# Optimization experiments

Measured on AMD Instinct MI355X. Metric: run time of the kernel, lower is better.

Reference implementation:

```python
import jax, jax.numpy as jnp
import numpy as np

N = 50000
E = 600000
IN_DIM = 256
H1, H2, H3 = 128, 64, 64
HEADS = 8


def _add_self_loops(edge_index, edge_weight=None):
    loop = jnp.arange(N, dtype=edge_index.dtype)
    src = jnp.concatenate([edge_index[0], loop])
    dst = jnp.concatenate([edge_index[1], loop])
    if edge_weight is None:
        return src, dst, None
    ew = jnp.concatenate([edge_weight, jnp.ones((N,), edge_weight.dtype)])
    return src, dst, ew


def gcn_conv(x, edge_index, edge_weight, W, b):
    # PyG GCNConv: add self-loops (weight 1), symmetric normalization, scatter-add.
    src, dst, ew = _add_self_loops(edge_index, edge_weight)
    deg = jax.ops.segment_sum(ew, dst, num_segments=N)          # [N]
    dinv = jnp.where(deg > 0, jax.lax.rsqrt(jnp.maximum(deg, 1e-12)), 0.0)
    coeff = dinv[src] * ew * dinv[dst]                          # [E+N]
    h = x @ W                                                    # [N, out]
    out = jax.ops.segment_sum(coeff[:, None] * h[src], dst, num_segments=N)
    return out + b


def gat_conv(x, edge_index, W, att_src, att_dst, b):
    # PyG GATConv, heads=HEADS, concat=False (mean over heads), leaky_relu slope 0.2.
    src, dst, _ = _add_self_loops(edge_index)
    C = W.shape[1] // HEADS
    h = (x @ W).reshape(N, HEADS, C)                             # [N,H,C]
    a_s = jnp.sum(h * att_src, axis=-1)                          # [N,H]
    a_d = jnp.sum(h * att_dst, axis=-1)                          # [N,H]
    e = jax.nn.leaky_relu(a_s[src] + a_d[dst], negative_slope=0.2)  # [E',H]
    # scatter-softmax over edges sharing a destination
    m = jax.ops.segment_max(e, dst, num_segments=N)              # [N,H]
    p = jnp.exp(e - m[dst])
    s = jax.ops.segment_sum(p, dst, num_segments=N)              # [N,H]
    alpha = p / (s[dst] + 1e-16)                                 # [E',H]
    out = jax.ops.segment_sum(alpha[:, :, None] * h[src], dst, num_segments=N)  # [N,H,C]
    return jnp.mean(out, axis=1) + b


def setup_inputs() -> dict:
    key = jax.random.key(0)
    ks = jax.random.split(key, 12)
    x = jax.random.normal(ks[0], (N, IN_DIM), dtype=jnp.float32)
    edge_index = jax.random.randint(ks[1], (2, E), 0, N, dtype=jnp.int32)
    edge_weight = jax.random.uniform(ks[2], (E,), dtype=jnp.float32)
    def glorot(k, shape):
        fan = shape[0] + shape[-1]
        return jax.random.normal(k, shape, dtype=jnp.float32) * np.sqrt(2.0 / fan)
    return {
        "x": x, "edge_index": edge_index, "edge_weight": edge_weight,
        "gc1_w": glorot(ks[3], (IN_DIM, H1)), "gc1_b": jnp.zeros((H1,), jnp.float32),
        "gat_w": glorot(ks[4], (H1, HEADS * H2)),
        "att_src": glorot(ks[5], (HEADS, H2)), "att_dst": glorot(ks[6], (HEADS, H2)),
        "gat_b": jnp.zeros((H2,), jnp.float32),
        "gc2_w": glorot(ks[7], (H2, H3)), "gc2_b": jnp.zeros((H3,), jnp.float32),
        "fc_w": glorot(ks[8], (H3, 1)), "fc_b": jnp.zeros((1,), jnp.float32),
    }


def reference(x, edge_index, edge_weight, gc1_w, gc1_b, gat_w, att_src, att_dst,
              gat_b, gc2_w, gc2_b, fc_w, fc_b):
    # dropout is inference no-op
    h = jax.nn.relu(gcn_conv(x, edge_index, edge_weight, gc1_w, gc1_b))
    h = jax.nn.relu(gat_conv(h, edge_index, gat_w, att_src, att_dst, gat_b))
    h = jax.nn.relu(gcn_conv(h, edge_index, edge_weight, gc2_w, gc2_b))
    return h @ fc_w + fc_b                                       # [N,1]
```

## Files before the change

kernel.cpp:

```cpp
#include <hip/hip_runtime.h>
#include <hip/hip_bf16.h>

#define GNN_N 50000
#define GNN_E 600000

typedef unsigned int uint;
typedef unsigned short ushort;
using short8 = __attribute__((ext_vector_type(8))) short;
using f32x4  = __attribute__((ext_vector_type(4))) float;

__device__ __forceinline__ float leaky02(float x) { return x > 0.f ? x : 0.2f * x; }
__device__ __forceinline__ ushort f2b(float f) {
    uint u = __float_as_uint(f);
    return (ushort)((u + 0x7fffu + ((u >> 16) & 1u)) >> 16);
}
__device__ __forceinline__ float b2f(ushort b) { return __uint_as_float(((uint)b) << 16); }
__device__ __forceinline__ float blo(uint u) { return __uint_as_float(u << 16); }
__device__ __forceinline__ float bhi(uint u) { return __uint_as_float(u & 0xffff0000u); }

__global__ void gnn_hist(const int* __restrict__ dst, const float* __restrict__ ew,
                         int* __restrict__ cnt, float* __restrict__ deg, int e) {
    int i = blockIdx.x * blockDim.x + threadIdx.x;
    if (i >= e) return;
    int d = dst[i];
    atomicAdd(&cnt[d], 1);
    atomicAdd(&deg[d], ew[i]);
}
__global__ void gnn_deg_fin(float* deg, int n) {
    int i = blockIdx.x * blockDim.x + threadIdx.x;
    if (i < n) deg[i] = rsqrtf(1.0f + deg[i]);
}
__global__ void gnn_scan1(const int* __restrict__ cnt, int* __restrict__ row_ptr,
                          int* __restrict__ blksum, int n) {
    __shared__ int sh[256];
    int tid = threadIdx.x;
    int base = blockIdx.x * 1024 + tid * 4;
    int v0 = (base + 0 < n) ? cnt[base + 0] : 0;
    int v1 = (base + 1 < n) ? cnt[base + 1] : 0;
    int v2 = (base + 2 < n) ? cnt[base + 2] : 0;
    int v3 = (base + 3 < n) ? cnt[base + 3] : 0;
    int tsum = v0 + v1 + v2 + v3;
    sh[tid] = tsum;
    __syncthreads();
    for (int off = 1; off < 256; off <<= 1) {
        int t = (tid >= off) ? sh[tid - off] : 0;
        __syncthreads();
        sh[tid] += t;
        __syncthreads();
    }
    int excl = sh[tid] - tsum;
    if (base + 0 < n) row_ptr[base + 0] = excl; excl += v0;
    if (base + 1 < n) row_ptr[base + 1] = excl; excl += v1;
    if (base + 2 < n) row_ptr[base + 2] = excl; excl += v2;
    if (base + 3 < n) row_ptr[base + 3] = excl;
    if (tid == 255) blksum[blockIdx.x] = sh[255];
}
__global__ void gnn_scan2(int* blksum, int nblk, int* row_ptr_end, int total) {
    if (threadIdx.x == 0 && blockIdx.x == 0) {
        int run = 0;
        for (int b = 0; b < nblk; ++b) { int t = blksum[b]; blksum[b] = run; run += t; }
        *row_ptr_end = total;
    }
}
__global__ void gnn_scan3(int* row_ptr, const int* __restrict__ blksum, int n) {
    int i = blockIdx.x * blockDim.x + threadIdx.x;
    if (i < n) row_ptr[i] += blksum[i >> 10];
}
__global__ void gnn_scatter(const int* __restrict__ src, const int* __restrict__ dst,
                            const float* __restrict__ ew, const float* __restrict__ dinv,
                            const int* __restrict__ row_ptr, int* __restrict__ fill,
                            int* __restrict__ esrc, float* __restrict__ ecw, int e) {
    int i = blockIdx.x * blockDim.x + threadIdx.x;
    if (i >= e) return;
    int d = dst[i];
    int s = src[i];
    int pos = row_ptr[d] + atomicAdd(&fill[d], 1);
    esrc[pos] = s;
    ecw[pos] = dinv[s] * ew[i] * dinv[d];
}

__global__ void gnn_prep(const float* __restrict__ gc1_w, const float* __restrict__ gat_w,
                         const float* __restrict__ gc2_w, const float* __restrict__ att_src,
                         const float* __restrict__ att_dst, ushort* __restrict__ w1t,
                         ushort* __restrict__ w2s_t, ushort* __restrict__ w3t,
                         float* __restrict__ wa_t) {
    int t = blockIdx.x * 256 + threadIdx.x;
    if (t < 32768) {
        int k = t >> 7, n = t & 127;
        w1t[n * 256 + k] = f2b(gc1_w[t]);
        return;
    }
    t -= 32768;
    if (t < 65536) {
        int c = t >> 10, r = t & 1023;
        int h = r >> 7, k = r & 127;
        w2s_t[t] = f2b(0.125f * gat_w[(size_t)k * 512 + h * 64 + c]);
        return;
    }
    t -= 65536;
    if (t < 4096) {
        int k = t >> 6, n = t & 63;
        w3t[n * 64 + k] = f2b(gc2_w[t]);
        return;
    }
    t -= 4096;
    if (t < 2048) {
        int j = t >> 7, k = t & 127;
        int h = j & 7;
        const float* av = (j < 8) ? att_src : att_dst;
        float s = 0.f;
        for (int c = 0; c < 64; ++c) s += gat_w[(size_t)k * 512 + h * 64 + c] * av[h * 64 + c];
        wa_t[j * 128 + k] = s;
    }
}

template <bool AF32, bool BIAS>
__global__ __launch_bounds__(256) void gnn_mfma_gemm(const void* __restrict__ Av,
                                                     const ushort* __restrict__ Bt,
                                                     ushort* __restrict__ C,
                                                     const float* __restrict__ bias,
                                                     int M, int N, int K) {
    __shared__ ushort As[64 * 40];
    __shared__ ushort Bs[64 * 40];
    const int tid = threadIdx.x;
    const int wv = tid >> 6, lane = tid & 63;
    const int g = lane >> 4, r = lane & 15;
    const int brow = blockIdx.y << 6, bcol = blockIdx.x << 6;

    const int srow = tid >> 2;
    const int skoff = (tid & 3) << 3;
    int arow = brow + srow;
    if (arow >= M) arow = M - 1;
    const ushort* A16 = (const ushort*)Av;
    const float*  A32 = (const float*)Av;
    const ushort* Ap16 = A16 + (size_t)arow * K + skoff;
    const float*  Ap32 = A32 + (size_t)arow * K + skoff;
    const ushort* Bp = Bt + (size_t)(bcol + srow) * K + skoff;
    ushort* AsW = &As[srow * 40 + skoff];
    ushort* BsW = &Bs[srow * 40 + skoff];

    f32x4 acc[4] = {};

    for (int k0 = 0; k0 < K; k0 += 32) {
        if constexpr (AF32) {
            float4 f0 = *(const float4*)(Ap32 + k0);
            float4 f1 = *(const float4*)(Ap32 + k0 + 4);
            short8 t;
            t[0] = (short)f2b(f0.x); t[1] = (short)f2b(f0.y);
            t[2] = (short)f2b(f0.z); t[3] = (short)f2b(f0.w);
            t[4] = (short)f2b(f1.x); t[5] = (short)f2b(f1.y);
            t[6] = (short)f2b(f1.z); t[7] = (short)f2b(f1.w);
            *(short8*)AsW = t;
        } else {
            *(short8*)AsW = *(const short8*)(Ap16 + k0);
        }
        *(short8*)BsW = *(const short8*)(Bp + k0);
        __syncthreads();
        short8 bfrag = *(const short8*)&Bs[(wv * 16 + r) * 40 + g * 8];
#pragma unroll
        for (int mb = 0; mb < 4; ++mb) {
            short8 afrag = *(const short8*)&As[(mb * 16 + r) * 40 + g * 8];
            acc[mb] = __builtin_amdgcn_mfma_f32_16x16x32_bf16(afrag, bfrag, acc[mb], 0, 0, 0);
        }
        __syncthreads();
    }

    const int col = bcol + wv * 16 + r;
    float bv = 0.f;
    if constexpr (BIAS) bv = bias[col];
#pragma unroll
    for (int mb = 0; mb < 4; ++mb) {
        int rowb = brow + mb * 16 + g * 4;
#pragma unroll
        for (int rr = 0; rr < 4; ++rr) {
            int row = rowb + rr;
            if (row < M) {
                float val = acc[mb][rr];
                if constexpr (BIAS) {
                    val += bv;
                    val = val > 0.f ? val : 0.f;
                }
                C[(size_t)row * N + col] = f2b(val);
            }
        }
    }
}

__global__ __launch_bounds__(256) void gnn_gcn_node128_asd(const int* __restrict__ row_ptr,
                                                           const int* __restrict__ esrc,
                                                           const float* __restrict__ ecw,
                                                           const float* __restrict__ dinv,
                                                           const ushort* __restrict__ hb,
                                                           const float* __restrict__ b,
                                                           const float* __restrict__ wa,
                                                           ushort* __restrict__ out,
                                                           float* __restrict__ a_s,
                                                           float* __restrict__ a_d, int n) {
    __shared__ float swa[16 * 128];
    for (int i = threadIdx.x; i < 16 * 128; i += 256) swa[i] = wa[i];
    __syncthreads();
    int v = blockIdx.x * 4 + (threadIdx.x >> 6);
    int lane = threadIdx.x & 63;
    if (v >= n) return;
    const int sl = lane & 31;
    const int half = lane >> 5;
    float di = dinv[v];
    float a0, a1, a2, a3;
    {
        float scl = half ? 0.f : di * di;
        uint2 u = *(const uint2*)(hb + (size_t)v * 128 + 4 * sl);
        a0 = scl * blo(u.x); a1 = scl * bhi(u.x);
        a2 = scl * blo(u.y); a3 = scl * bhi(u.y);
    }
    int beg = row_ptr[v], end = row_ptr[v + 1];
    int cntE = end - beg;
    int pairs = cntE >> 1;
    int i = 0;
    for (; i + 4 <= pairs; i += 4) {
        int s[4]; float c[4]; uint2 u[4];
#pragma unroll
        for (int t = 0; t < 4; ++t) s[t] = esrc[beg + 2 * (i + t) + half];
#pragma unroll
        for (int t = 0; t < 4; ++t) c[t] = ecw[beg + 2 * (i + t) + half];
#pragma unroll
        for (int t = 0; t < 4; ++t) u[t] = *(const uint2*)(hb + (size_t)s[t] * 128 + 4 * sl);
#pragma unroll
        for (int t = 0; t < 4; ++t) {
            a0 += c[t] * blo(u[t].x); a1 += c[t] * bhi(u[t].x);
            a2 += c[t] * blo(u[t].y); a3 += c[t] * bhi(u[t].y);
        }
    }
    for (; i < pairs; ++i) {
        int s = esrc[beg + 2 * i + half];
        float c = ecw[beg + 2 * i + half];
        uint2 u = *(const uint2*)(hb + (size_t)s * 128 + 4 * sl);
        a0 += c * blo(u.x); a1 += c * bhi(u.x);
        a2 += c * blo(u.y); a3 += c * bhi(u.y);
    }
    if (cntE & 1) {
        int s = esrc[end - 1];
        float c = half ? 0.f : ecw[end - 1];
        uint2 u = *(const uint2*)(hb + (size_t)s * 128 + 4 * sl);
        a0 += c * blo(u.x); a1 += c * bhi(u.x);
        a2 += c * blo(u.y); a3 += c * bhi(u.y);
    }
    a0 += __shfl_xor(a0, 32); a1 += __shfl_xor(a1, 32);
    a2 += __shfl_xor(a2, 32); a3 += __shfl_xor(a3, 32);

    float4 bv = *(const float4*)(b + 4 * sl);
    float o0 = a0 + bv.x, o1 = a1 + bv.y, o2 = a2 + bv.z, o3 = a3 + bv.w;
    o0 = o0 > 0.f ? o0 : 0.f; o1 = o1 > 0.f ? o1 : 0.f;
    o2 = o2 > 0.f ? o2 : 0.f; o3 = o3 > 0.f ? o3 : 0.f;
    if (lane < 32) {
        uint2 w;
        w.x = (uint)f2b(o0) | ((uint)f2b(o1) << 16);
        w.y = (uint)f2b(o2) | ((uint)f2b(o3) << 16);
        *(uint2*)(out + (size_t)v * 128 + 4 * sl) = w;
    }

    float part[16];
#pragma unroll
    for (int j = 0; j < 16; ++j) {
        const float* wj = &swa[j * 128 + 4 * sl];
        part[j] = o0 * wj[0] + o1 * wj[1] + o2 * wj[2] + o3 * wj[3];
    }
#pragma unroll
    for (int m = 1; m < 32; m <<= 1) {
#pragma unroll
        for (int j = 0; j < 16; ++j) part[j] += __shfl_xor(part[j], m);
    }
    if (lane == 0) {
#pragma unroll
        for (int j = 0; j < 8; ++j) {
            a_s[(size_t)v * 8 + j] = part[j];
            a_d[(size_t)v * 8 + j] = part[8 + j];
        }
    }
}

__global__ __launch_bounds__(256) void gnn_gat_z(const int* __restrict__ row_ptr,
                                                 const int* __restrict__ esrc,
                                                 const float* __restrict__ a_s,
                                                 const float* __restrict__ a_d,
                                                 const ushort* __restrict__ g1b,
                                                 ushort* __restrict__ zb, int n) {
    int v = blockIdx.x * 4 + (threadIdx.x >> 6);
    int lane = threadIdx.x & 63;
    if (v >= n) return;
    const int sl = lane & 31;
    const int half = lane >> 5;
    const int hh = lane & 7;
    const int hbase = lane & 32;
    const float adh = a_d[(size_t)v * 8 + hh];

    float z0[8] = {}, z1[8] = {}, z2[8] = {}, z3[8] = {};
    float sloc = 0.f;
    {
        float pv = __expf(leaky02(a_s[(size_t)v * 8 + hh] + adh));
        if (half) pv = 0.f;
        sloc += pv;
        uint2 u = *(const uint2*)(g1b + (size_t)v * 128 + 4 * sl);
        float g0 = blo(u.x), g1v = bhi(u.x), g2v = blo(u.y), g3v = bhi(u.y);
        float ph[8];
#pragma unroll
        for (int h = 0; h < 8; ++h) ph[h] = __shfl(pv, hbase | h);
#pragma unroll
        for (int h = 0; h < 8; ++h) {
            z0[h] += ph[h] * g0; z1[h] += ph[h] * g1v;
            z2[h] += ph[h] * g2v; z3[h] += ph[h] * g3v;
        }
    }
    int beg = row_ptr[v], end = row_ptr[v + 1];
    int cntE = end - beg;
    int pairs = cntE >> 1;
    int i = 0;
    for (; i + 2 <= pairs; i += 2) {
        int s[2]; float e[2]; uint2 u[2];
#pragma unroll
        for (int t = 0; t < 2; ++t) s[t] = esrc[beg + 2 * (i + t) + half];
#pragma unroll
        for (int t = 0; t < 2; ++t) e[t] = a_s[(size_t)s[t] * 8 + hh];
#pragma unroll
        for (int t = 0; t < 2; ++t) u[t] = *(const uint2*)(g1b + (size_t)s[t] * 128 + 4 * sl);
#pragma unroll
        for (int t = 0; t < 2; ++t) {
            float pv = __expf(leaky02(e[t] + adh));
            sloc += pv;
            float g0 = blo(u[t].x), g1v = bhi(u[t].x), g2v = blo(u[t].y), g3v = bhi(u[t].y);
            float ph[8];
#pragma unroll
            for (int h = 0; h < 8; ++h) ph[h] = __shfl(pv, hbase | h);
#pragma unroll
            for (int h = 0; h < 8; ++h) {
                z0[h] += ph[h] * g0; z1[h] += ph[h] * g1v;
                z2[h] += ph[h] * g2v; z3[h] += ph[h] * g3v;
            }
        }
    }
    for (; i < pairs; ++i) {
        int s = esrc[beg + 2 * i + half];
        float pv = __expf(leaky02(a_s[(size_t)s * 8 + hh] + adh));
        sloc += pv;
        uint2 u = *(const uint2*)(g1b + (size_t)s * 128 + 4 * sl);
        float g0 = blo(u.x), g1v = bhi(u.x), g2v = blo(u.y), g3v = bhi(u.y);
        float ph[8];
#pragma unroll
        for (int h = 0; h < 8; ++h) ph[h] = __shfl(pv, hbase | h);
#pragma unroll
        for (int h = 0; h < 8; ++h) {
            z0[h] += ph[h] * g0; z1[h] += ph[h] * g1v;
            z2[h] += ph[h] * g2v; z3[h] += ph[h] * g3v;
        }
    }
    if (cntE & 1) {
        int s = esrc[end - 1];
        float pv = __expf(leaky02(a_s[(size_t)s * 8 + hh] + adh));
        if (half) pv = 0.f;
        sloc += pv;
        uint2 u = *(const uint2*)(g1b + (size_t)s * 128 + 4 * sl);
        float g0 = blo(u.x), g1v = bhi(u.x), g2v = blo(u.y), g3v = bhi(u.y);
        float ph[8];
#pragma unroll
        for (int h = 0; h < 8; ++h) ph[h] = __shfl(pv, hbase | h);
#pragma unroll
        for (int h = 0; h < 8; ++h) {
            z0[h] += ph[h] * g0; z1[h] += ph[h] * g1v;
            z2[h] += ph[h] * g2v; z3[h] += ph[h] * g3v;
        }
    }
    float slx = sloc + __shfl_xor(sloc, 32) + 1e-16f;
#pragma unroll
    for (int h = 0; h < 8; ++h) {
        z0[h] += __shfl_xor(z0[h], 32); z1[h] += __shfl_xor(z1[h], 32);
        z2[h] += __shfl_xor(z2[h], 32); z3[h] += __shfl_xor(z3[h], 32);
    }
    if (lane < 32) {
#pragma unroll
        for (int h = 0; h < 8; ++h) {
            float rs = 1.f / __shfl(slx, h);
            uint2 w;
            w.x = (uint)f2b(z0[h] * rs) | ((uint)f2b(z1[h] * rs) << 16);
            w.y = (uint)f2b(z2[h] * rs) | ((uint)f2b(z3[h] * rs) << 16);
            *(uint2*)(zb + (size_t)v * 1024 + h * 128 + 4 * sl) = w;
        }
    }
}

__global__ __launch_bounds__(256) void gnn_gcn_node64_fc(const int* __restrict__ row_ptr,
                                                         const int* __restrict__ esrc,
                                                         const float* __restrict__ ecw,
                                                         const float* __restrict__ dinv,
                                                         const ushort* __restrict__ hb,
                                                         const float* __restrict__ b,
                                                         const float* __restrict__ fc_w,
                                                         const float* __restrict__ fc_b,
                                                         float* __restrict__ out, int n) {
    int v = blockIdx.x * 4 + (threadIdx.x >> 6);
    int lane = threadIdx.x & 63;
    if (v >= n) return;
    const int sl = lane & 31;
    const int half = lane >> 5;
    float di = dinv[v];
    float a0, a1;
    {
        float scl = half ? 0.f : di * di;
        uint u = *(const uint*)(hb + (size_t)v * 64 + 2 * sl);
        a0 = scl * blo(u); a1 = scl * bhi(u);
    }
    int beg = row_ptr[v], end = row_ptr[v + 1];
    int cntE = end - beg;
    int pairs = cntE >> 1;
    int i = 0;
    for (; i + 4 <= pairs; i += 4) {
        int s[4]; float c[4]; uint u[4];
#pragma unroll
        for (int t = 0; t < 4; ++t) s[t] = esrc[beg + 2 * (i + t) + half];
#pragma unroll
        for (int t = 0; t < 4; ++t) c[t] = ecw[beg + 2 * (i + t) + half];
#pragma unroll
        for (int t = 0; t < 4; ++t) u[t] = *(const uint*)(hb + (size_t)s[t] * 64 + 2 * sl);
#pragma unroll
        for (int t = 0; t < 4; ++t) { a0 += c[t] * blo(u[t]); a1 += c[t] * bhi(u[t]); }
    }
    for (; i < pairs; ++i) {
        int s = esrc[beg + 2 * i + half];
        float c = ecw[beg + 2 * i + half];
        uint u = *(const uint*)(hb + (size_t)s * 64 + 2 * sl);
        a0 += c * blo(u); a1 += c * bhi(u);
    }
    if (cntE & 1) {
        int s = esrc[end - 1];
        float c = half ? 0.f : ecw[end - 1];
        uint u = *(const uint*)(hb + (size_t)s * 64 + 2 * sl);
        a0 += c * blo(u); a1 += c * bhi(u);
    }
    a0 += __shfl_xor(a0, 32);
    a1 += __shfl_xor(a1, 32);
    float o0 = a0 + b[2 * sl];
    float o1 = a1 + b[2 * sl + 1];
    o0 = o0 > 0.f ? o0 : 0.f;
    o1 = o1 > 0.f ? o1 : 0.f;
    float val = o0 * fc_w[2 * sl] + o1 * fc_w[2 * sl + 1];
#pragma unroll
    for (int m = 1; m < 32; m <<= 1) val += __shfl_xor(val, m);
    if (lane == 0) out[v] = val + fc_b[0];
}

extern "C" void kernel_launch(void* const* d_in, const int* in_sizes, int n_in,
                              void* d_out, int out_size, void* d_ws, size_t ws_size,
                              hipStream_t stream) {
    const float* x       = (const float*)d_in[0];
    const int*   ei      = (const int*)d_in[1];
    const float* ew      = (const float*)d_in[2];
    const float* gc1_w   = (const float*)d_in[3];
    const float* gc1_b   = (const float*)d_in[4];
    const float* gat_w   = (const float*)d_in[5];
    const float* att_src = (const float*)d_in[6];
    const float* att_dst = (const float*)d_in[7];
    const float* gat_b   = (const float*)d_in[8];
    const float* gc2_w   = (const float*)d_in[9];
    const float* gc2_b   = (const float*)d_in[10];
    const float* fc_w    = (const float*)d_in[11];
    const float* fc_b    = (const float*)d_in[12];
    float* out = (float*)d_out;

    const int N = GNN_N;
    const int E = in_sizes[2];
    const int* src = ei;
    const int* dst = ei + E;

    char* p = (char*)d_ws;
    ushort* zb  = (ushort*)p; p += (size_t)N * 1024 * 2;
    ushort* h1b = (ushort*)p; p += (size_t)N * 128 * 2;
    ushort* g1b = (ushort*)p; p += (size_t)N * 128 * 2;
    ushort* g2b = (ushort*)p; p += (size_t)N * 64 * 2;
    ushort* h3b = (ushort*)p; p += (size_t)N * 64 * 2;
    ushort* w1t = (ushort*)p; p += (size_t)128 * 256 * 2;
    ushort* w2s_t = (ushort*)p; p += (size_t)64 * 1024 * 2;
    ushort* w3t = (ushort*)p; p += (size_t)64 * 64 * 2;
    float*  wa_t = (float*)p; p += 16 * 128 * 4;
    float*  a_s = (float*)p;  p += (size_t)N * 8 * 4;
    float*  a_d = (float*)p;  p += (size_t)N * 8 * 4;
    int* row_ptr = (int*)p;   p += (size_t)(N + 64) * 4;
    int* esrc = (int*)p;      p += (size_t)E * 4;
    float* ecw = (float*)p;   p += (size_t)E * 4;
    int* cnt = (int*)p;       p += (size_t)N * 4;
    int* fill = (int*)p;      p += (size_t)N * 4;
    float* dinv = (float*)p;  p += (size_t)N * 4;
    int* blksum = (int*)p;    p += 4096;

    auto cdiv = [](long a, long b) { return (int)((a + b - 1) / b); };

    hipMemsetAsync(cnt, 0, (size_t)N * 12, stream);
    gnn_hist<<<cdiv(E, 256), 256, 0, stream>>>(dst, ew, cnt, dinv, E);
    gnn_deg_fin<<<cdiv(N, 256), 256, 0, stream>>>(dinv, N);
    const int nblk = cdiv(N, 1024);
    gnn_scan1<<<nblk, 256, 0, stream>>>(cnt, row_ptr, blksum, N);
    gnn_scan2<<<1, 64, 0, stream>>>(blksum, nblk, row_ptr + N, E);
    gnn_scan3<<<cdiv(N, 256), 256, 0, stream>>>(row_ptr, blksum, N);
    gnn_scatter<<<cdiv(E, 256), 256, 0, stream>>>(src, dst, ew, dinv, row_ptr, fill, esrc, ecw, E);

    gnn_prep<<<408, 256, 0, stream>>>(gc1_w, gat_w, gc2_w, att_src, att_dst, w1t, w2s_t, w3t, wa_t);

    {
        dim3 grid(128 / 64, cdiv(N, 64));
        gnn_mfma_gemm<true, false><<<grid, 256, 0, stream>>>(x, w1t, h1b, nullptr, N, 128, 256);
    }
    gnn_gcn_node128_asd<<<cdiv(N, 4), 256, 0, stream>>>(row_ptr, esrc, ecw, dinv, h1b, gc1_b,
                                                        wa_t, g1b, a_s, a_d, N);

    gnn_gat_z<<<cdiv(N, 4), 256, 0, stream>>>(row_ptr, esrc, a_s, a_d, g1b, zb, N);
    {
        dim3 grid(1, cdiv(N, 64));
        gnn_mfma_gemm<false, true><<<grid, 256, 0, stream>>>(zb, w2s_t, g2b, gat_b, N, 64, 1024);
    }

    {
        dim3 grid(1, cdiv(N, 64));
        gnn_mfma_gemm<false, false><<<grid, 256, 0, stream>>>(g2b, w3t, h3b, nullptr, N, 64, 64);
    }
    gnn_gcn_node64_fc<<<cdiv(N, 4), 256, 0, stream>>>(row_ptr, esrc, ecw, dinv, h3b, gc2_b,
                                                      fc_w, fc_b, out, N);
}
```

Baseline: 338.3 us.

## Sort CSR edge order per node for deterministic degree and aggregation

Replaces the float atomic degree accumulation with a per-node pass that sorts edge indices within each destination segment and sums weights in a fixed order. Edge coefficients and sources are then written in that sorted order by a separate kernel. This makes the CSR build deterministic, at the cost of two extra kernels, an extra index buffer, and serial per-thread insertion sorts.

```diff
diff --git a/kernel.cpp b/kernel.cpp
--- a/kernel.cpp
+++ b/kernel.cpp
@@ -18,17 +18,9 @@
 __device__ __forceinline__ float blo(uint u) { return __uint_as_float(u << 16); }
 __device__ __forceinline__ float bhi(uint u) { return __uint_as_float(u & 0xffff0000u); }
 
-__global__ void gnn_hist(const int* __restrict__ dst, const float* __restrict__ ew,
-                         int* __restrict__ cnt, float* __restrict__ deg, int e) {
+__global__ void gnn_hist(const int* __restrict__ dst, int* __restrict__ cnt, int e) {
     int i = blockIdx.x * blockDim.x + threadIdx.x;
-    if (i >= e) return;
-    int d = dst[i];
-    atomicAdd(&cnt[d], 1);
-    atomicAdd(&deg[d], ew[i]);
-}
-__global__ void gnn_deg_fin(float* deg, int n) {
-    int i = blockIdx.x * blockDim.x + threadIdx.x;
-    if (i < n) deg[i] = rsqrtf(1.0f + deg[i]);
+    if (i < e) atomicAdd(&cnt[dst[i]], 1);
 }
 __global__ void gnn_scan1(const int* __restrict__ cnt, int* __restrict__ row_ptr,
                           int* __restrict__ blksum, int n) {
@@ -66,17 +58,54 @@
     int i = blockIdx.x * blockDim.x + threadIdx.x;
     if (i < n) row_ptr[i] += blksum[i >> 10];
 }
-__global__ void gnn_scatter(const int* __restrict__ src, const int* __restrict__ dst,
-                            const float* __restrict__ ew, const float* __restrict__ dinv,
-                            const int* __restrict__ row_ptr, int* __restrict__ fill,
-                            int* __restrict__ esrc, float* __restrict__ ecw, int e) {
+__global__ void gnn_scatter_idx(const int* __restrict__ dst, const int* __restrict__ row_ptr,
+                                int* __restrict__ fill, int* __restrict__ tord, int e) {
     int i = blockIdx.x * blockDim.x + threadIdx.x;
     if (i >= e) return;
     int d = dst[i];
+    int pos = row_ptr[d] + atomicAdd(&fill[d], 1);
+    tord[pos] = i;
+}
+__global__ void gnn_sortdeg(const float* __restrict__ ew, int* __restrict__ tord,
+                            const int* __restrict__ row_ptr, float* __restrict__ dinv, int n) {
+    int v = blockIdx.x * blockDim.x + threadIdx.x;
+    if (v >= n) return;
+    int beg = row_ptr[v], end = row_ptr[v + 1];
+    int d = end - beg;
+    if (d <= 64) {
+        int buf[64];
+        for (int i = 0; i < d; ++i) buf[i] = tord[beg + i];
+        for (int i = 1; i < d; ++i) {
+            int key = buf[i];
+            int k = i - 1;
+            while (k >= 0 && buf[k] > key) { buf[k + 1] = buf[k]; --k; }
+            buf[k + 1] = key;
+        }
+        float s = 1.f;
+        for (int i = 0; i < d; ++i) { tord[beg + i] = buf[i]; s += ew[buf[i]]; }
+        dinv[v] = rsqrtf(s);
+    } else {
+        for (int i = beg + 1; i < end; ++i) {
+            int key = tord[i];
+            int k = i - 1;
+            while (k >= beg && tord[k] > key) { tord[k + 1] = tord[k]; --k; }
+            tord[k + 1] = key;
+        }
+        float s = 1.f;
+        for (int i = beg; i < end; ++i) s += ew[tord[i]];
+        dinv[v] = rsqrtf(s);
+    }
+}
+__global__ void gnn_edgefin(const int* __restrict__ src, const int* __restrict__ dst,
+                            const float* __restrict__ ew, const float* __restrict__ dinv,
+                            const int* __restrict__ tord, int* __restrict__ esrc,
+                            float* __restrict__ ecw, int e) {
+    int pos = blockIdx.x * blockDim.x + threadIdx.x;
+    if (pos >= e) return;
+    int i = tord[pos];
     int s = src[i];
-    int pos = row_ptr[d] + atomicAdd(&fill[d], 1);
     esrc[pos] = s;
-    ecw[pos] = dinv[s] * ew[i] * dinv[d];
+    ecw[pos] = dinv[s] * ew[i] * dinv[dst[i]];
 }
 
 __global__ void gnn_prep(const float* __restrict__ gc1_w, const float* __restrict__ gat_w,
@@ -484,6 +513,7 @@
     int* row_ptr = (int*)p;   p += (size_t)(N + 64) * 4;
     int* esrc = (int*)p;      p += (size_t)E * 4;
     float* ecw = (float*)p;   p += (size_t)E * 4;
+    int* tord = (int*)p;      p += (size_t)E * 4;
     int* cnt = (int*)p;       p += (size_t)N * 4;
     int* fill = (int*)p;      p += (size_t)N * 4;
     float* dinv = (float*)p;  p += (size_t)N * 4;
@@ -491,14 +521,15 @@
 
     auto cdiv = [](long a, long b) { return (int)((a + b - 1) / b); };
 
-    hipMemsetAsync(cnt, 0, (size_t)N * 12, stream);
-    gnn_hist<<<cdiv(E, 256), 256, 0, stream>>>(dst, ew, cnt, dinv, E);
-    gnn_deg_fin<<<cdiv(N, 256), 256, 0, stream>>>(dinv, N);
+    hipMemsetAsync(cnt, 0, (size_t)N * 8, stream);
+    gnn_hist<<<cdiv(E, 256), 256, 0, stream>>>(dst, cnt, E);
     const int nblk = cdiv(N, 1024);
     gnn_scan1<<<nblk, 256, 0, stream>>>(cnt, row_ptr, blksum, N);
     gnn_scan2<<<1, 64, 0, stream>>>(blksum, nblk, row_ptr + N, E);
     gnn_scan3<<<cdiv(N, 256), 256, 0, stream>>>(row_ptr, blksum, N);
-    gnn_scatter<<<cdiv(E, 256), 256, 0, stream>>>(src, dst, ew, dinv, row_ptr, fill, esrc, ecw, E);
+    gnn_scatter_idx<<<cdiv(E, 256), 256, 0, stream>>>(dst, row_ptr, fill, tord, E);
+    gnn_sortdeg<<<cdiv(N, 256), 256, 0, stream>>>(ew, tord, row_ptr, dinv, N);
+    gnn_edgefin<<<cdiv(E, 256), 256, 0, stream>>>(src, dst, ew, dinv, tord, esrc, ecw, E);
 
     gnn_prep<<<408, 256, 0, stream>>>(gc1_w, gat_w, gc2_w, att_src, att_dst, w1t, w2s_t, w3t, wa_t);
 
```

After: 363.3 us. 7.4% more time.
